# Kernel optimization log

Measured on AMD Instinct MI355X. Metric: run time of the kernel, lower is better.

## Reference

```python
import jax, jax.numpy as jnp
import numpy as np

TEMP = 0.07
BASE_TEMP = 0.07
BANK = 8192
B = 512      # samples per view; features has 2*B rows
D = 128      # feature dim
N_CLASSES = 100


def _l2norm(x, axis=-1):
    return x / jnp.linalg.norm(x, axis=axis, keepdims=True)


def setup_inputs() -> dict:
    key = jax.random.key(0)
    k1, k2, k3, k4, k5 = jax.random.split(key, 5)
    # SupCon features are L2-normalized embeddings; two views stacked: [2B, 1, D]
    features = _l2norm(jax.random.normal(k1, (2 * B, 1, D), jnp.float32))
    label = jax.random.randint(k2, (B,), 0, N_CLASSES)
    # memory banks stored as [D, bank_size] (lightly MemoryBankModule layout)
    bank1 = _l2norm(jax.random.normal(k3, (D, BANK), jnp.float32), axis=0)
    bank2 = _l2norm(jax.random.normal(k4, (D, BANK), jnp.float32), axis=0)
    bank_labels = jax.random.randint(k5, (BANK,), 0, N_CLASSES)
    return {"features": features, "label": label, "bank1": bank1,
            "bank2": bank2, "bank_labels": bank_labels}


def _branch_loss(cf, pos_mask, neg_mask):
    # cf: [N, D] anchor==contrast features
    logits = jnp.matmul(cf, cf.T) / TEMP                       # [N, N]
    logits = logits - jax.lax.stop_gradient(logits.max(axis=1, keepdims=True))
    # denominator: sum of exp(logits) over NEGATIVES only (square(mask-1) mask)
    denom = jnp.log((jnp.exp(logits) * neg_mask).sum(axis=1, keepdims=True))
    log_prob = logits - denom                                  # [N, N]
    mean_log_prob_pos = (pos_mask * log_prob).sum(axis=1) / pos_mask.sum(axis=1)
    return -(TEMP / BASE_TEMP) * mean_log_prob_pos             # [N]


def reference(features, label, bank1, bank2, bank_labels):
    d = features.shape[-1]
    fr = features.reshape(-1, d)                # [2B, D]
    nb = fr.shape[0] // 2
    f1, f2 = fr[:nb], fr[nb:]                   # [B, D] each

    labels_all = jnp.concatenate([bank_labels.reshape(-1, 1),
                                  label.reshape(-1, 1)], axis=0)   # [N, 1]
    same = (labels_all == labels_all.T)                            # [N, N]
    mask = same.astype(fr.dtype)
    n = mask.shape[0]
    self_mask = 1.0 - jnp.eye(n, dtype=fr.dtype)
    pos_mask = mask * self_mask                 # positives excluding self
    neg_mask = jnp.square(mask - 1.0)           # 1 where labels differ

    cf1 = jnp.concatenate([bank2.T, f1], axis=0)   # [N, D]
    cf2 = jnp.concatenate([bank1.T, f2], axis=0)   # [N, D]

    class_loss = (_branch_loss(cf1, pos_mask, neg_mask)
                  + _branch_loss(cf2, pos_mask, neg_mask)) / 2.0
    loss = class_loss.mean()
    return (loss, loss, loss)
```

## Files before the change

### kernel.cpp

```cpp
#include <hip/hip_runtime.h>
#include <math.h>

#define NTOT 8704
#define BANKN 8192
#define NB 512
#define DIM 128
#define INVT (1.0f / 0.07f)
#define NCHUNK 8
#define TPC 17
#define BN 64

using short8 = __attribute__((ext_vector_type(8))) short;
using f32x4 = __attribute__((ext_vector_type(4))) float;

static __device__ __forceinline__ ushort f2bf(float f) {
  union { float f; unsigned u; } v;
  v.f = f;
  unsigned r = v.u + 0x7fffu + ((v.u >> 16) & 1u);
  return (ushort)(r >> 16);
}

__global__ void pack_bank_kernel(const float* __restrict__ bank1,
                                 const float* __restrict__ bank2,
                                 ushort* __restrict__ cf1b,
                                 ushort* __restrict__ cf2b) {
  const float* src = (blockIdx.z == 0) ? bank2 : bank1;
  ushort* dst = (blockIdx.z == 0) ? cf1b : cf2b;
  __shared__ float tile[32][33];
  int tx = threadIdx.x, ty = threadIdx.y;
  int bx = blockIdx.x, by = blockIdx.y;
  int col = bx * 32 + tx;
#pragma unroll
  for (int s = 0; s < 32; s += 8)
    tile[ty + s][tx] = src[(by * 32 + ty + s) * BANKN + col];
  __syncthreads();
  int k = by * 32 + tx;
#pragma unroll
  for (int s = 0; s < 32; s += 8)
    dst[(size_t)(bx * 32 + ty + s) * DIM + k] = f2bf(tile[tx][ty + s]);
}

__global__ void pack_feat_kernel(const float* __restrict__ feats,
                                 ushort* __restrict__ cf1b,
                                 ushort* __restrict__ cf2b) {
  int t = blockIdx.x * blockDim.x + threadIdx.x;
  const int total = (2 * NB * DIM) / 4;
  if (t < total) {
    float4 v = reinterpret_cast<const float4*>(feats)[t];
    ushort4 o;
    o.x = f2bf(v.x); o.y = f2bf(v.y); o.z = f2bf(v.z); o.w = f2bf(v.w);
    const int half = total / 2;
    if (t < half)
      reinterpret_cast<ushort4*>(cf1b + (size_t)BANKN * DIM)[t] = o;
    else
      reinterpret_cast<ushort4*>(cf2b + (size_t)BANKN * DIM)[t - half] = o;
  }
}

__global__ void pack_lab_kernel(const int* __restrict__ bank_labels,
                                const int* __restrict__ label,
                                int* __restrict__ lab_all,
                                int* __restrict__ cnt) {
  __shared__ int h[100];
  const int tid = threadIdx.x;
  if (tid < 100) h[tid] = 0;
  __syncthreads();
  for (int i = tid; i < NTOT; i += 256) {
    const int v = (i < BANKN) ? bank_labels[i] : label[i - BANKN];
    lab_all[i] = v;
    atomicAdd(&h[v], 1);
  }
  __syncthreads();
  if (tid < 100) cnt[tid] = h[tid];
}

__global__ __launch_bounds__(256) void supcon_mfma_kernel(
    const ushort* __restrict__ cf1b, const ushort* __restrict__ cf2b,
    const int* __restrict__ lab_all, float* __restrict__ partials) {
  const int rb = blockIdx.x;
  const int chunk = blockIdx.y;
  const int branch = blockIdx.z;
  const ushort* __restrict__ cf = branch ? cf2b : cf1b;

  const int tid = threadIdx.x;
  const int wid = tid >> 6, lane = tid & 63;
  const int l15 = lane & 15, l4 = lane >> 4;
  const int rowW = rb * 128 + wid * 32;

  __shared__ ushort Bt[2][BN * DIM];

  short8 a[2][4];
#pragma unroll
  for (int rt = 0; rt < 2; ++rt) {
    const int r = rowW + rt * 16 + l15;
#pragma unroll
    for (int ks = 0; ks < 4; ++ks)
      a[rt][ks] = *reinterpret_cast<const short8*>(cf + (size_t)r * DIM + ks * 32 + l4 * 8);
  }
  int rlab[2][4];
#pragma unroll
  for (int rt = 0; rt < 2; ++rt)
#pragma unroll
    for (int rg = 0; rg < 4; ++rg)
      rlab[rt][rg] = lab_all[rowW + rt * 16 + l4 * 4 + rg];

  float Zr[2][4] = {{0.f, 0.f, 0.f, 0.f}, {0.f, 0.f, 0.f, 0.f}};
  float Pr[2][4] = {{0.f, 0.f, 0.f, 0.f}, {0.f, 0.f, 0.f, 0.f}};

  auto STAGE = [&](int t, int buf) {
    const int col0 = (chunk * TPC + t) * BN;
#pragma unroll
    for (int it = 0; it < 4; ++it) {
      const int o = it * 256 + tid;
      const int row = o >> 4, cc = o & 15;
      const ushort* src = cf + (size_t)(col0 + row) * DIM + ((cc ^ (row & 7)) * 8);
      ushort* dst = &Bt[buf][(it * 256 + wid * 64) * 8];
      __builtin_amdgcn_global_load_lds(
          (const __attribute__((address_space(1))) void*)src,
          (__attribute__((address_space(3))) void*)dst, 16, 0, 0);
    }
  };

  STAGE(0, 0);
  asm volatile("s_waitcnt vmcnt(0)" ::: "memory");
  __syncthreads();

  const float c2 = INVT;
  int cur = 0;
  for (int t = 0; t < TPC; ++t) {
    if (t + 1 < TPC) STAGE(t + 1, cur ^ 1);

    const int col0 = (chunk * TPC + t) * BN;
    int clab[4];
#pragma unroll
    for (int ct = 0; ct < 4; ++ct) clab[ct] = lab_all[col0 + ct * 16 + l15];

    f32x4 acc[2][4];
#pragma unroll
    for (int rt = 0; rt < 2; ++rt)
#pragma unroll
      for (int ct = 0; ct < 4; ++ct) acc[rt][ct] = (f32x4){0.f, 0.f, 0.f, 0.f};

#pragma unroll
    for (int ks = 0; ks < 4; ++ks) {
      short8 b[4];
#pragma unroll
      for (int ct = 0; ct < 4; ++ct) {
        const int r = ct * 16 + l15;
        const int swz = (ks * 4 + l4) ^ (r & 7);
        b[ct] = *reinterpret_cast<const short8*>(&Bt[cur][r * DIM + swz * 8]);
      }
#pragma unroll
      for (int rt = 0; rt < 2; ++rt)
#pragma unroll
        for (int ct = 0; ct < 4; ++ct)
          acc[rt][ct] = __builtin_amdgcn_mfma_f32_16x16x32_bf16(
              a[rt][ks], b[ct], acc[rt][ct], 0, 0, 0);
    }

#pragma unroll
    for (int ct = 0; ct < 4; ++ct) {
      const int cl = clab[ct];
#pragma unroll
      for (int rt = 0; rt < 2; ++rt)
#pragma unroll
        for (int rg = 0; rg < 4; ++rg) {
          const float v = acc[rt][ct][rg];
          const float e = __expf(fmaf(v, c2, -c2));
          const bool same = (rlab[rt][rg] == cl);
          Zr[rt][rg] += same ? 0.0f : e;
          Pr[rt][rg] += same ? v : 0.0f;
        }
    }

    asm volatile("s_waitcnt vmcnt(0)" ::: "memory");
    __syncthreads();
    cur ^= 1;
  }

#pragma unroll
  for (int rt = 0; rt < 2; ++rt)
#pragma unroll
    for (int rg = 0; rg < 4; ++rg) {
      float z = Zr[rt][rg], p = Pr[rt][rg];
#pragma unroll
      for (int off = 1; off < 16; off <<= 1) {
        z += __shfl_xor(z, off);
        p += __shfl_xor(p, off);
      }
      if (l15 == 0) {
        const int row = rowW + rt * 16 + l4 * 4 + rg;
        const size_t base = (size_t)(branch * NCHUNK + chunk) * 2 * NTOT;
        partials[base + row] = z;
        partials[base + NTOT + row] = p;
      }
    }
}

__global__ void loss_part_kernel(const float* __restrict__ partials,
                                 const int* __restrict__ lab_all,
                                 const int* __restrict__ cnt,
                                 float* __restrict__ red) {
  const int bx = blockIdx.x, branch = blockIdx.y;
  const int tid = threadIdx.x;
  float local = 0.f;
  if (tid < 128) {
    const int row = bx * 128 + tid;
    float z = 0.f, p = 0.f;
    for (int ch = 0; ch < NCHUNK; ++ch) {
      const size_t base = (size_t)(branch * NCHUNK + ch) * 2 * NTOT;
      z += partials[base + row];
      p += partials[base + NTOT + row];
    }
    const float C = (float)(cnt[lab_all[row]] - 1);
    const float denom = INVT + logf(z);
    local = -((INVT * (p - 1.0f)) / C - denom);
  }
  __shared__ float s[256];
  s[tid] = local;
  __syncthreads();
  for (int st = 128; st > 0; st >>= 1) {
    if (tid < st) s[tid] += s[tid + st];
    __syncthreads();
  }
  if (tid == 0) red[branch * 68 + bx] = s[0];
}

__global__ void loss_final_kernel(const float* __restrict__ red,
                                  float* __restrict__ out) {
  const int tid = threadIdx.x;
  __shared__ float s[256];
  s[tid] = (tid < 136) ? red[tid] : 0.f;
  __syncthreads();
  for (int st = 128; st > 0; st >>= 1) {
    if (tid < st) s[tid] += s[tid + st];
    __syncthreads();
  }
  if (tid == 0) {
    const float v = s[0] / (2.0f * NTOT);
    out[0] = v; out[1] = v; out[2] = v;
  }
}

extern "C" void kernel_launch(void* const* d_in, const int* in_sizes, int n_in,
                              void* d_out, int out_size, void* d_ws,
                              size_t ws_size, hipStream_t stream) {
  const float* features = (const float*)d_in[0];
  const int* label = (const int*)d_in[1];
  const float* bank1 = (const float*)d_in[2];
  const float* bank2 = (const float*)d_in[3];
  const int* bank_labels = (const int*)d_in[4];
  float* out = (float*)d_out;

  char* ws = (char*)d_ws;
  ushort* cf1b = (ushort*)(ws);
  ushort* cf2b = (ushort*)(ws + 2228224);
  int* lab_all = (int*)(ws + 4456448);
  int* cnt = (int*)(ws + 4491264);
  float* partials = (float*)(ws + 4491776);
  float* red = (float*)(ws + 5605888);

  pack_bank_kernel<<<dim3(BANKN / 32, DIM / 32, 2), dim3(32, 8), 0, stream>>>(
      bank1, bank2, cf1b, cf2b);
  pack_feat_kernel<<<dim3((2 * NB * DIM / 4 + 255) / 256), dim3(256), 0,
                     stream>>>(features, cf1b, cf2b);
  pack_lab_kernel<<<dim3(1), dim3(256), 0, stream>>>(bank_labels, label,
                                                     lab_all, cnt);

  supcon_mfma_kernel<<<dim3(NTOT / 128, NCHUNK, 2), dim3(256), 0, stream>>>(
      cf1b, cf2b, lab_all, partials);

  loss_part_kernel<<<dim3(68, 2), dim3(256), 0, stream>>>(partials, lab_all,
                                                          cnt, red);
  loss_final_kernel<<<dim3(1), dim3(256), 0, stream>>>(red, out);
}
```

Before: 154.4 us.

## Sort rows by label to specialize same/different-class tiles and fuse pack kernels

Rows are counting-sorted by label in a prep kernel so that each class occupies a contiguous column range. Tiles lying wholly outside or inside a warp's class range can then skip the per-element label compare and select. The separate pack kernels are merged into one gather-and-convert kernel that also zeroes the accumulators. Per-chunk partials are replaced by float atomics, which lets the loss reduction collapse into a single kernel. In exchange the bank reads become strided gathers, the prep kernel is serial and single-block, the atomics make summation order nondeterministic, and exp is computed as a prescaled exp2.

```diff
diff --git a/kernel.cpp b/kernel.cpp
--- a/kernel.cpp
+++ b/kernel.cpp
@@ -6,11 +6,13 @@
 #define NB 512
 #define DIM 128
 #define INVT (1.0f / 0.07f)
+#define C2L 20.6099131801f
 #define NCHUNK 8
 #define TPC 17
 #define BN 64
 
 using short8 = __attribute__((ext_vector_type(8))) short;
+using ushort8 = __attribute__((ext_vector_type(8))) unsigned short;
 using f32x4 = __attribute__((ext_vector_type(4))) float;
 
 static __device__ __forceinline__ ushort f2bf(float f) {
@@ -20,63 +22,94 @@
   return (ushort)(r >> 16);
 }
 
-__global__ void pack_bank_kernel(const float* __restrict__ bank1,
-                                 const float* __restrict__ bank2,
-                                 ushort* __restrict__ cf1b,
-                                 ushort* __restrict__ cf2b) {
-  const float* src = (blockIdx.z == 0) ? bank2 : bank1;
-  ushort* dst = (blockIdx.z == 0) ? cf1b : cf2b;
-  __shared__ float tile[32][33];
-  int tx = threadIdx.x, ty = threadIdx.y;
-  int bx = blockIdx.x, by = blockIdx.y;
-  int col = bx * 32 + tx;
-#pragma unroll
-  for (int s = 0; s < 32; s += 8)
-    tile[ty + s][tx] = src[(by * 32 + ty + s) * BANKN + col];
-  __syncthreads();
-  int k = by * 32 + tx;
-#pragma unroll
-  for (int s = 0; s < 32; s += 8)
-    dst[(size_t)(bx * 32 + ty + s) * DIM + k] = f2bf(tile[tx][ty + s]);
-}
-
-__global__ void pack_feat_kernel(const float* __restrict__ feats,
-                                 ushort* __restrict__ cf1b,
-                                 ushort* __restrict__ cf2b) {
-  int t = blockIdx.x * blockDim.x + threadIdx.x;
-  const int total = (2 * NB * DIM) / 4;
-  if (t < total) {
-    float4 v = reinterpret_cast<const float4*>(feats)[t];
-    ushort4 o;
-    o.x = f2bf(v.x); o.y = f2bf(v.y); o.z = f2bf(v.z); o.w = f2bf(v.w);
-    const int half = total / 2;
-    if (t < half)
-      reinterpret_cast<ushort4*>(cf1b + (size_t)BANKN * DIM)[t] = o;
-    else
-      reinterpret_cast<ushort4*>(cf2b + (size_t)BANKN * DIM)[t - half] = o;
-  }
-}
-
-__global__ void pack_lab_kernel(const int* __restrict__ bank_labels,
-                                const int* __restrict__ label,
-                                int* __restrict__ lab_all,
-                                int* __restrict__ cnt) {
-  __shared__ int h[100];
+static __device__ __forceinline__ float fast_exp2(float x) {
+#if __has_builtin(__builtin_amdgcn_exp2f)
+  return __builtin_amdgcn_exp2f(x);
+#else
+  return exp2f(x);
+#endif
+}
+
+__global__ void prep_kernel(const int* __restrict__ bank_labels,
+                            const int* __restrict__ label,
+                            int* __restrict__ rowmap, int* __restrict__ lo,
+                            int* __restrict__ hi) {
+  __shared__ int h[101];
+  __shared__ int st[101];
+  __shared__ int cur[100];
   const int tid = threadIdx.x;
-  if (tid < 100) h[tid] = 0;
+  if (tid < 101) h[tid] = 0;
   __syncthreads();
   for (int i = tid; i < NTOT; i += 256) {
     const int v = (i < BANKN) ? bank_labels[i] : label[i - BANKN];
-    lab_all[i] = v;
     atomicAdd(&h[v], 1);
   }
   __syncthreads();
-  if (tid < 100) cnt[tid] = h[tid];
+  if (tid == 0) {
+    int s = 0;
+    for (int c = 0; c < 100; ++c) { st[c] = s; s += h[c]; }
+    st[100] = s;
+  }
+  __syncthreads();
+  if (tid < 100) cur[tid] = st[tid];
+  __syncthreads();
+  for (int i = tid; i < NTOT; i += 256) {
+    const int v = (i < BANKN) ? bank_labels[i] : label[i - BANKN];
+    const int p = atomicAdd(&cur[v], 1);
+    rowmap[p] = i;
+    lo[p] = st[v];
+    hi[p] = st[v + 1];
+  }
+}
+
+__global__ void pack_kernel(const float* __restrict__ features,
+                            const float* __restrict__ bank1,
+                            const float* __restrict__ bank2,
+                            const int* __restrict__ rowmap,
+                            ushort* __restrict__ cf1b,
+                            ushort* __restrict__ cf2b,
+                            float* __restrict__ zp ) {
+  const int tid = threadIdx.x;
+  const int branch = blockIdx.y;
+  const int gid = (blockIdx.y * 136 + blockIdx.x) * 256 + tid;
+  if (gid < (4 * NTOT) / 4)
+    reinterpret_cast<float4*>(zp)[gid] = make_float4(0.f, 0.f, 0.f, 0.f);
+
+  const int r = blockIdx.x * 64 + (tid >> 2);
+  const int kq = tid & 3;
+  const int o = rowmap[r];
+  ushort tmp[32];
+  if (o < BANKN) {
+    const float* __restrict__ bank = branch ? bank1 : bank2;
+#pragma unroll
+    for (int kk = 0; kk < 32; ++kk)
+      tmp[kk] = f2bf(bank[(size_t)(kq * 32 + kk) * BANKN + o]);
+  } else {
+    const float* __restrict__ f =
+        features + (size_t)((o - BANKN) + (branch ? NB : 0)) * DIM + kq * 32;
+#pragma unroll
+    for (int q = 0; q < 8; ++q) {
+      float4 v = reinterpret_cast<const float4*>(f)[q];
+      tmp[q * 4 + 0] = f2bf(v.x);
+      tmp[q * 4 + 1] = f2bf(v.y);
+      tmp[q * 4 + 2] = f2bf(v.z);
+      tmp[q * 4 + 3] = f2bf(v.w);
+    }
+  }
+  ushort* dst = (branch ? cf2b : cf1b) + (size_t)r * DIM + kq * 32;
+#pragma unroll
+  for (int q = 0; q < 4; ++q) {
+    ushort8 w;
+#pragma unroll
+    for (int j = 0; j < 8; ++j) w[j] = tmp[q * 8 + j];
+    *reinterpret_cast<ushort8*>(dst + q * 8) = w;
+  }
 }
 
 __global__ __launch_bounds__(256) void supcon_mfma_kernel(
     const ushort* __restrict__ cf1b, const ushort* __restrict__ cf2b,
-    const int* __restrict__ lab_all, float* __restrict__ partials) {
+    const int* __restrict__ lo, const int* __restrict__ hi,
+    float* __restrict__ zp) {
   const int rb = blockIdx.x;
   const int chunk = blockIdx.y;
   const int branch = blockIdx.z;
@@ -97,12 +130,19 @@
     for (int ks = 0; ks < 4; ++ks)
       a[rt][ks] = *reinterpret_cast<const short8*>(cf + (size_t)r * DIM + ks * 32 + l4 * 8);
   }
-  int rlab[2][4];
+  int rlo[2][4], rhi[2][4];
 #pragma unroll
   for (int rt = 0; rt < 2; ++rt)
 #pragma unroll
-    for (int rg = 0; rg < 4; ++rg)
-      rlab[rt][rg] = lab_all[rowW + rt * 16 + l4 * 4 + rg];
+    for (int rg = 0; rg < 4; ++rg) {
+      const int rr = rowW + rt * 16 + l4 * 4 + rg;
+      rlo[rt][rg] = lo[rr];
+      rhi[rt][rg] = hi[rr];
+    }
+  const int u_lo = lo[rowW];
+  const int u_hi = hi[rowW + 31];
+  const int lo_last = lo[rowW + 31];
+  const int hi_first = hi[rowW];
 
   float Zr[2][4] = {{0.f, 0.f, 0.f, 0.f}, {0.f, 0.f, 0.f, 0.f}};
   float Pr[2][4] = {{0.f, 0.f, 0.f, 0.f}, {0.f, 0.f, 0.f, 0.f}};
@@ -113,7 +153,8 @@
     for (int it = 0; it < 4; ++it) {
       const int o = it * 256 + tid;
       const int row = o >> 4, cc = o & 15;
-      const ushort* src = cf + (size_t)(col0 + row) * DIM + ((cc ^ (row & 7)) * 8);
+      const ushort* src =
+          cf + (size_t)(col0 + row) * DIM + ((cc ^ (row & 7)) * 8);
       ushort* dst = &Bt[buf][(it * 256 + wid * 64) * 8];
       __builtin_amdgcn_global_load_lds(
           (const __attribute__((address_space(1))) void*)src,
@@ -125,15 +166,11 @@
   asm volatile("s_waitcnt vmcnt(0)" ::: "memory");
   __syncthreads();
 
-  const float c2 = INVT;
   int cur = 0;
   for (int t = 0; t < TPC; ++t) {
     if (t + 1 < TPC) STAGE(t + 1, cur ^ 1);
 
     const int col0 = (chunk * TPC + t) * BN;
-    int clab[4];
-#pragma unroll
-    for (int ct = 0; ct < 4; ++ct) clab[ct] = lab_all[col0 + ct * 16 + l15];
 
     f32x4 acc[2][4];
 #pragma unroll
@@ -158,19 +195,36 @@
               a[rt][ks], b[ct], acc[rt][ct], 0, 0, 0);
     }
 
-#pragma unroll
-    for (int ct = 0; ct < 4; ++ct) {
-      const int cl = clab[ct];
-#pragma unroll
-      for (int rt = 0; rt < 2; ++rt)
-#pragma unroll
-        for (int rg = 0; rg < 4; ++rg) {
-          const float v = acc[rt][ct][rg];
-          const float e = __expf(fmaf(v, c2, -c2));
-          const bool same = (rlab[rt][rg] == cl);
-          Zr[rt][rg] += same ? 0.0f : e;
-          Pr[rt][rg] += same ? v : 0.0f;
-        }
+    if (col0 + BN <= u_lo || col0 >= u_hi) {
+#pragma unroll
+      for (int ct = 0; ct < 4; ++ct)
+#pragma unroll
+        for (int rt = 0; rt < 2; ++rt)
+#pragma unroll
+          for (int rg = 0; rg < 4; ++rg)
+            Zr[rt][rg] += fast_exp2(fmaf(acc[rt][ct][rg], C2L, -C2L));
+    } else if (col0 >= lo_last && col0 + BN <= hi_first) {
+#pragma unroll
+      for (int ct = 0; ct < 4; ++ct)
+#pragma unroll
+        for (int rt = 0; rt < 2; ++rt)
+#pragma unroll
+          for (int rg = 0; rg < 4; ++rg) Pr[rt][rg] += acc[rt][ct][rg];
+    } else {
+#pragma unroll
+      for (int ct = 0; ct < 4; ++ct) {
+        const int c = col0 + ct * 16 + l15;
+#pragma unroll
+        for (int rt = 0; rt < 2; ++rt)
+#pragma unroll
+          for (int rg = 0; rg < 4; ++rg) {
+            const float v = acc[rt][ct][rg];
+            const float e = fast_exp2(fmaf(v, C2L, -C2L));
+            const bool s = (c >= rlo[rt][rg]) && (c < rhi[rt][rg]);
+            Zr[rt][rg] += s ? 0.0f : e;
+            Pr[rt][rg] += s ? v : 0.0f;
+          }
+      }
     }
 
     asm volatile("s_waitcnt vmcnt(0)" ::: "memory");
@@ -178,6 +232,8 @@
     cur ^= 1;
   }
 
+  float* Zrow = zp;
+  float* Prow = zp + 2 * NTOT;
 #pragma unroll
   for (int rt = 0; rt < 2; ++rt)
 #pragma unroll
@@ -190,47 +246,30 @@
       }
       if (l15 == 0) {
         const int row = rowW + rt * 16 + l4 * 4 + rg;
-        const size_t base = (size_t)(branch * NCHUNK + chunk) * 2 * NTOT;
-        partials[base + row] = z;
-        partials[base + NTOT + row] = p;
+        atomicAdd(&Zrow[branch * NTOT + row], z);
+        atomicAdd(&Prow[branch * NTOT + row], p);
       }
     }
 }
 
-__global__ void loss_part_kernel(const float* __restrict__ partials,
-                                 const int* __restrict__ lab_all,
-                                 const int* __restrict__ cnt,
-                                 float* __restrict__ red) {
-  const int bx = blockIdx.x, branch = blockIdx.y;
+__global__ void loss_kernel(const float* __restrict__ zp,
+                            const int* __restrict__ lo,
+                            const int* __restrict__ hi,
+                            float* __restrict__ out) {
   const int tid = threadIdx.x;
+  const float* Zrow = zp;
+  const float* Prow = zp + 2 * NTOT;
   float local = 0.f;
-  if (tid < 128) {
-    const int row = bx * 128 + tid;
-    float z = 0.f, p = 0.f;
-    for (int ch = 0; ch < NCHUNK; ++ch) {
-      const size_t base = (size_t)(branch * NCHUNK + ch) * 2 * NTOT;
-      z += partials[base + row];
-      p += partials[base + NTOT + row];
-    }
-    const float C = (float)(cnt[lab_all[row]] - 1);
+  for (int idx = tid; idx < 2 * NTOT; idx += 256) {
+    const int row = (idx >= NTOT) ? idx - NTOT : idx;
+    const float z = Zrow[idx];
+    const float p = Prow[idx];
+    const float C = (float)(hi[row] - lo[row] - 1);
     const float denom = INVT + logf(z);
-    local = -((INVT * (p - 1.0f)) / C - denom);
+    local += -((INVT * (p - 1.0f)) / C - denom);
   }
   __shared__ float s[256];
   s[tid] = local;
-  __syncthreads();
-  for (int st = 128; st > 0; st >>= 1) {
-    if (tid < st) s[tid] += s[tid + st];
-    __syncthreads();
-  }
-  if (tid == 0) red[branch * 68 + bx] = s[0];
-}
-
-__global__ void loss_final_kernel(const float* __restrict__ red,
-                                  float* __restrict__ out) {
-  const int tid = threadIdx.x;
-  __shared__ float s[256];
-  s[tid] = (tid < 136) ? red[tid] : 0.f;
   __syncthreads();
   for (int st = 128; st > 0; st >>= 1) {
     if (tid < st) s[tid] += s[tid + st];
@@ -255,22 +294,16 @@
   char* ws = (char*)d_ws;
   ushort* cf1b = (ushort*)(ws);
   ushort* cf2b = (ushort*)(ws + 2228224);
-  int* lab_all = (int*)(ws + 4456448);
-  int* cnt = (int*)(ws + 4491264);
-  float* partials = (float*)(ws + 4491776);
-  float* red = (float*)(ws + 5605888);
-
-  pack_bank_kernel<<<dim3(BANKN / 32, DIM / 32, 2), dim3(32, 8), 0, stream>>>(
-      bank1, bank2, cf1b, cf2b);
-  pack_feat_kernel<<<dim3((2 * NB * DIM / 4 + 255) / 256), dim3(256), 0,
-                     stream>>>(features, cf1b, cf2b);
-  pack_lab_kernel<<<dim3(1), dim3(256), 0, stream>>>(bank_labels, label,
-                                                     lab_all, cnt);
-
+  int* rowmap = (int*)(ws + 4456448);
+  int* lo = (int*)(ws + 4491264);
+  int* hi = (int*)(ws + 4526080);
+  float* zp = (float*)(ws + 4560896);
+
+  prep_kernel<<<dim3(1), dim3(256), 0, stream>>>(bank_labels, label, rowmap,
+                                                 lo, hi);
+  pack_kernel<<<dim3(NTOT / 64, 2), dim3(256), 0, stream>>>(
+      features, bank1, bank2, rowmap, cf1b, cf2b, zp);
   supcon_mfma_kernel<<<dim3(NTOT / 128, NCHUNK, 2), dim3(256), 0, stream>>>(
-      cf1b, cf2b, lab_all, partials);
-
-  loss_part_kernel<<<dim3(68, 2), dim3(256), 0, stream>>>(partials, lab_all,
-                                                          cnt, red);
-  loss_final_kernel<<<dim3(1), dim3(256), 0, stream>>>(red, out);
-}
+      cf1b, cf2b, lo, hi, zp);
+  loss_kernel<<<dim3(1), dim3(256), 0, stream>>>(zp, lo, hi, out);
+}
```

Result: slower. 201.1 us (+30.2%).
